# Kernel optimization log

Hardware: AMD Instinct MI355X
Metric: run time of the kernel (lower is better)

The kernel has to match this reference:

```python
import jax, jax.numpy as jnp
import numpy as np

N = 50000   # nodes
E = 800000  # edges (avg degree 16)
D0 = 256    # input feat dim
H1, D1 = 4, 64  # layer1 heads, per-head dim
H2, D2 = 4, 64  # layer2 heads, per-head dim
NEG_SLOPE = 0.2


def setup_inputs() -> dict:
    key = jax.random.key(0)
    ks = jax.random.split(key, 9)
    s = 0.1
    feature = jax.random.normal(ks[0], (N, D0), jnp.float32)
    src = jax.random.randint(ks[1], (E,), 0, N, dtype=jnp.int32)
    dst = jax.random.randint(ks[2], (E,), 0, N, dtype=jnp.int32)
    W1 = jax.random.normal(ks[3], (D0, H1 * D1), jnp.float32) * s
    al1 = jax.random.normal(ks[4], (H1, D1), jnp.float32) * s
    ar1 = jax.random.normal(ks[5], (H1, D1), jnp.float32) * s
    W2 = jax.random.normal(ks[6], (H1 * D1, H2 * D2), jnp.float32) * s
    al2 = jax.random.normal(ks[7], (H2, D2), jnp.float32) * s
    ar2 = jax.random.normal(ks[8], (H2, D2), jnp.float32) * s
    return dict(feature=feature, W1=W1, al1=al1, ar1=ar1,
                W2=W2, al2=al2, ar2=ar2, src=src, dst=dst)


def gat_conv(x, W, al, ar, src, dst, H, d, act):
    # x: [N, in]; W: [in, H*d]; al, ar: [H, d]
    feat = (x @ W).reshape(N, H, d)                 # [N,H,d]
    el = jnp.einsum('nhd,hd->nh', feat, al)         # [N,H] src-side score
    er = jnp.einsum('nhd,hd->nh', feat, ar)         # [N,H] dst-side score
    e = jax.nn.leaky_relu(el[src] + er[dst], NEG_SLOPE)  # [E,H]
    # segment softmax over edges grouped by destination node
    m = jax.ops.segment_max(e, dst, num_segments=N)      # [N,H]
    ex = jnp.exp(e - m[dst])                             # [E,H]
    denom = jax.ops.segment_sum(ex, dst, num_segments=N) # [N,H]
    alpha = ex / jnp.maximum(denom[dst], 1e-9)           # [E,H]
    msg = feat[src] * alpha[..., None]                   # [E,H,d]
    out = jax.ops.segment_sum(msg, dst, num_segments=N)  # [N,H,d]
    return act(out)


def reference(feature, W1, al1, ar1, W2, al2, ar2, src, dst):
    h = gat_conv(feature, W1, al1, ar1, src, dst, H1, D1, jax.nn.elu)  # [N,H1,D1]
    h = h.reshape(N, H1 * D1)                                          # concat heads
    h = gat_conv(h, W2, al2, ar2, src, dst, H2, D2, lambda x: x)       # [N,H2,D2]
    return h.mean(axis=1)                                              # mean over heads -> [N,D2]
```

## Files before the change

kernel.cpp:

```cpp
#include <hip/hip_runtime.h>
#include <hip/hip_fp16.h>
#include <math.h>
#include <stdint.h>

#define NNODES 50000
#define NEDGES 800000
#define DIM 256
#define HEADS 4
#define DH 64
#define NEG_SLOPE 0.2f

#define CSR_NPB 1024
#define CSR_NB ((NNODES + CSR_NPB - 1) / CSR_NPB)

typedef _Float16 half8 __attribute__((ext_vector_type(8)));
typedef float floatx4 __attribute__((ext_vector_type(4)));

static __device__ __forceinline__ float h2f(unsigned short h) {
  __half x = *(const __half*)&h;
  return __half2float(x);
}
static __device__ __forceinline__ unsigned short f2h(float f) {
  __half x = __float2half(f);
  return *(const unsigned short*)&x;
}

__global__ __launch_bounds__(256) void wt_k(const float* __restrict__ W1,
                                            const float* __restrict__ W2,
                                            _Float16* __restrict__ WT1,
                                            _Float16* __restrict__ WT2) {
  int b = blockIdx.x;
  const float* W = (b < 256) ? W1 : W2;
  _Float16* WT = (b < 256) ? WT1 : WT2;
  int n = b & 255;
  int k = threadIdx.x;
  WT[n * 256 + k] = (_Float16)W[k * 256 + n];
}

template <typename AT>
__global__ __launch_bounds__(256) void gemm_k(const AT* __restrict__ A,
                                              const _Float16* __restrict__ BT,
                                              const float* __restrict__ alw,
                                              const float* __restrict__ arw,
                                              unsigned short* __restrict__ Cb,
                                              float* __restrict__ el,
                                              float* __restrict__ er, int M) {
  __shared__ __attribute__((aligned(16))) _Float16 Asl[64][72];
  __shared__ __attribute__((aligned(16))) _Float16 Bsl[256][72];
  int t = threadIdx.x;
  int lane = t & 63, w = t >> 6;
  int m16 = lane & 15, q = lane >> 4;
  int row0 = blockIdx.x * 64;
  floatx4 acc[4][4];
#pragma unroll
  for (int i = 0; i < 4; ++i)
#pragma unroll
    for (int j = 0; j < 4; ++j) acc[i][j] = (floatx4){0.f, 0.f, 0.f, 0.f};

  float4 alv[4], arv[4];
#pragma unroll
  for (int ni = 0; ni < 4; ++ni) {
    alv[ni] = *(const float4*)&alw[w * 64 + ni * 16 + q * 4];
    arv[ni] = *(const float4*)&arw[w * 64 + ni * 16 + q * 4];
  }

  int arow = t >> 2, akoff = (t & 3) * 16;

  for (int k0 = 0; k0 < DIM; k0 += 64) {
    if constexpr (sizeof(AT) == 4) {
      float4 x0 = make_float4(0.f, 0.f, 0.f, 0.f), x1 = x0, x2 = x0, x3 = x0;
      if (row0 + arow < M) {
        const float* ap = (const float*)&A[(size_t)(row0 + arow) * DIM + k0 + akoff];
        x0 = *(const float4*)ap;
        x1 = *(const float4*)(ap + 4);
        x2 = *(const float4*)(ap + 8);
        x3 = *(const float4*)(ap + 12);
      }
      half8 h0, h1;
      h0[0] = (_Float16)x0.x; h0[1] = (_Float16)x0.y;
      h0[2] = (_Float16)x0.z; h0[3] = (_Float16)x0.w;
      h0[4] = (_Float16)x1.x; h0[5] = (_Float16)x1.y;
      h0[6] = (_Float16)x1.z; h0[7] = (_Float16)x1.w;
      h1[0] = (_Float16)x2.x; h1[1] = (_Float16)x2.y;
      h1[2] = (_Float16)x2.z; h1[3] = (_Float16)x2.w;
      h1[4] = (_Float16)x3.x; h1[5] = (_Float16)x3.y;
      h1[6] = (_Float16)x3.z; h1[7] = (_Float16)x3.w;
      *(half8*)&Asl[arow][akoff] = h0;
      *(half8*)&Asl[arow][akoff + 8] = h1;
    } else {
      int4 x0 = make_int4(0, 0, 0, 0), x1 = x0;
      if (row0 + arow < M) {
        const AT* ap = &A[(size_t)(row0 + arow) * DIM + k0 + akoff];
        x0 = *(const int4*)ap;
        x1 = *(const int4*)(ap + 8);
      }
      *(int4*)&Asl[arow][akoff] = x0;
      *(int4*)&Asl[arow][akoff + 8] = x1;
    }
    {
      const _Float16* bp = &BT[(size_t)t * 256 + k0];
#pragma unroll
      for (int c = 0; c < 8; ++c)
        *(int4*)&Bsl[t][c * 8] = *(const int4*)(bp + c * 8);
    }
    __syncthreads();
    half8 wf[2][4], af[2][4];
#pragma unroll
    for (int s = 0; s < 2; ++s)
#pragma unroll
      for (int i = 0; i < 4; ++i) {
        wf[s][i] = *(const half8*)&Bsl[w * 64 + i * 16 + m16][s * 32 + q * 8];
        af[s][i] = *(const half8*)&Asl[i * 16 + m16][s * 32 + q * 8];
      }
#pragma unroll
    for (int s = 0; s < 2; ++s)
#pragma unroll
      for (int mi = 0; mi < 4; ++mi)
#pragma unroll
        for (int ni = 0; ni < 4; ++ni)
          acc[mi][ni] = __builtin_amdgcn_mfma_f32_16x16x32_f16(
              wf[s][ni], af[s][mi], acc[mi][ni], 0, 0, 0);
    __syncthreads();
  }

#pragma unroll
  for (int mi = 0; mi < 4; ++mi) {
    int node = row0 + mi * 16 + m16;
    float pl = 0.f, pr = 0.f;
#pragma unroll
    for (int ni = 0; ni < 4; ++ni) {
      pl += acc[mi][ni][0] * alv[ni].x + acc[mi][ni][1] * alv[ni].y +
            acc[mi][ni][2] * alv[ni].z + acc[mi][ni][3] * alv[ni].w;
      pr += acc[mi][ni][0] * arv[ni].x + acc[mi][ni][1] * arv[ni].y +
            acc[mi][ni][2] * arv[ni].z + acc[mi][ni][3] * arv[ni].w;
    }
    pl += __shfl_xor(pl, 16, 64); pl += __shfl_xor(pl, 32, 64);
    pr += __shfl_xor(pr, 16, 64); pr += __shfl_xor(pr, 32, 64);
    if (q == 0 && node < M) {
      el[node * HEADS + w] = pl;
      er[node * HEADS + w] = pr;
    }
    if (node < M) {
#pragma unroll
      for (int ni = 0; ni < 4; ++ni) {
        ushort4 o;
        o.x = f2h(acc[mi][ni][0]); o.y = f2h(acc[mi][ni][1]);
        o.z = f2h(acc[mi][ni][2]); o.w = f2h(acc[mi][ni][3]);
        *(ushort4*)&Cb[(size_t)node * DIM + w * 64 + ni * 16 + q * 4] = o;
      }
    }
  }
}

__global__ __launch_bounds__(256) void deg_k(const int* __restrict__ dst,
                                             int* __restrict__ deg) {
  int e8 = (blockIdx.x * 256 + threadIdx.x) * 8;
  if (e8 < NEDGES) {
    int4 d0 = *(const int4*)&dst[e8];
    int4 d1 = *(const int4*)&dst[e8 + 4];
    atomicAdd(&deg[d0.x], 1);
    atomicAdd(&deg[d0.y], 1);
    atomicAdd(&deg[d0.z], 1);
    atomicAdd(&deg[d0.w], 1);
    atomicAdd(&deg[d1.x], 1);
    atomicAdd(&deg[d1.y], 1);
    atomicAdd(&deg[d1.z], 1);
    atomicAdd(&deg[d1.w], 1);
  }
}

__global__ __launch_bounds__(256) void csr_part_k(const int* __restrict__ deg,
                                                  int* __restrict__ bsum) {
  __shared__ int ws[4];
  int t = threadIdx.x, lane = t & 63, w = t >> 6;
  int idx = blockIdx.x * CSR_NPB + t * 4;
  int s = 0;
  if (idx < NNODES) {
    int4 v = *(const int4*)&deg[idx];
    s = v.x + v.y + v.z + v.w;
  }
#pragma unroll
  for (int off = 1; off < 64; off <<= 1) s += __shfl_xor(s, off, 64);
  if (lane == 0) ws[w] = s;
  __syncthreads();
  if (t == 0) bsum[blockIdx.x] = ws[0] + ws[1] + ws[2] + ws[3];
}

__global__ __launch_bounds__(64) void csr_mid_k(const int* __restrict__ bsum,
                                                int* __restrict__ bbase,
                                                int* __restrict__ row_ptr) {
  int t = threadIdx.x;
  int v = (t < CSR_NB) ? bsum[t] : 0;
  int incl = v;
#pragma unroll
  for (int off = 1; off < 64; off <<= 1) {
    int u = __shfl_up(incl, off, 64);
    if (t >= off) incl += u;
  }
  if (t < CSR_NB) bbase[t] = incl - v;
  if (t == 0) row_ptr[NNODES] = NEDGES;
}

__global__ __launch_bounds__(256) void csr_emit_k(const int* __restrict__ deg,
                                                  const int* __restrict__ bbase,
                                                  int* __restrict__ row_ptr,
                                                  int* __restrict__ cursor) {
  __shared__ int ws[4];
  int t = threadIdx.x, lane = t & 63, w = t >> 6;
  int idx = blockIdx.x * CSR_NPB + t * 4;
  int4 v = make_int4(0, 0, 0, 0);
  if (idx < NNODES) v = *(const int4*)&deg[idx];
  int s0 = v.x, s1 = s0 + v.y, s2 = s1 + v.z, s3 = s2 + v.w;
  int incl = s3;
#pragma unroll
  for (int off = 1; off < 64; off <<= 1) {
    int u = __shfl_up(incl, off, 64);
    if (lane >= off) incl += u;
  }
  if (lane == 63) ws[w] = incl;
  __syncthreads();
  int wbase = 0;
#pragma unroll
  for (int i = 0; i < 4; ++i)
    if (i < w) wbase += ws[i];
  int base = bbase[blockIdx.x] + wbase + incl - s3;
  if (idx < NNODES) {
    int4 rp = make_int4(base, base + s0, base + s1, base + s2);
    *(int4*)&row_ptr[idx] = rp;
    *(int4*)&cursor[idx] = rp;
  }
}

__global__ __launch_bounds__(256) void scatter_k(const int* __restrict__ src,
                                                 const int* __restrict__ dst,
                                                 int* __restrict__ cursor,
                                                 int* __restrict__ srcoff) {
  int e8 = (blockIdx.x * 256 + threadIdx.x) * 8;
  if (e8 < NEDGES) {
    int4 s0 = *(const int4*)&src[e8];
    int4 s1 = *(const int4*)&src[e8 + 4];
    int4 d0 = *(const int4*)&dst[e8];
    int4 d1 = *(const int4*)&dst[e8 + 4];
    int p0 = atomicAdd(&cursor[d0.x], 1);
    int p1 = atomicAdd(&cursor[d0.y], 1);
    int p2 = atomicAdd(&cursor[d0.z], 1);
    int p3 = atomicAdd(&cursor[d0.w], 1);
    int p4 = atomicAdd(&cursor[d1.x], 1);
    int p5 = atomicAdd(&cursor[d1.y], 1);
    int p6 = atomicAdd(&cursor[d1.z], 1);
    int p7 = atomicAdd(&cursor[d1.w], 1);
    srcoff[p0] = s0.x << 9;
    srcoff[p1] = s0.y << 9;
    srcoff[p2] = s0.z << 9;
    srcoff[p3] = s0.w << 9;
    srcoff[p4] = s1.x << 9;
    srcoff[p5] = s1.y << 9;
    srcoff[p6] = s1.z << 9;
    srcoff[p7] = s1.w << 9;
  }
}

template <int MODE>
__global__ __launch_bounds__(256) void agg_k(const unsigned short* __restrict__ feat,
                                             const float* __restrict__ el,
                                             const float* __restrict__ er,
                                             const int* __restrict__ row_ptr,
                                             const int* __restrict__ srcoff,
                                             void* __restrict__ outp) {
  int lane = threadIdx.x & 63;
  int w = threadIdx.x >> 6;
  int n = blockIdx.x * 4 + w;
  if (n >= NNODES) return;
  int h = lane >> 4;
  int hsel = lane & 3;
  int esel = lane >> 2;
  int beg = row_ptr[n], end = row_ptr[n + 1];
  float erv = er[n * HEADS + hsel];
  int laneByte = lane * 8;
  const char* fb = (const char*)feat;
  const char* elb = (const char*)el;
  float a0 = 0.f, a1 = 0.f, a2 = 0.f, a3 = 0.f, sume = 0.f;
  for (int c0 = beg; c0 < end; c0 += 16) {
    int soff = 0;
    if (lane < 16 && c0 + lane < end) soff = srcoff[c0 + lane];
    float av = 0.f;
    if (c0 + esel < end) {
      int sE = __shfl(soff, esel, 64);
      float elv = *(const float*)(elb + (sE >> 5) + hsel * 4);
      float v = elv + erv;
      v = v > 0.f ? v : NEG_SLOPE * v;
      av = __expf(v);
    }
#pragma unroll
    for (int j = 0; j < 16; ++j) {
      int sB = __shfl(soff, j, 64);
      float a = __shfl(av, 4 * j + h, 64);
      ushort4 u = *(const ushort4*)(fb + (sB + laneByte));
      a0 += h2f(u.x) * a;
      a1 += h2f(u.y) * a;
      a2 += h2f(u.z) * a;
      a3 += h2f(u.w) * a;
      sume += a;
    }
  }
  float inv = 1.f / fmaxf(sume, 1e-9f);
  a0 *= inv; a1 *= inv; a2 *= inv; a3 *= inv;
  if (MODE == 1) {
    a0 = a0 > 0.f ? a0 : (__expf(a0) - 1.f);
    a1 = a1 > 0.f ? a1 : (__expf(a1) - 1.f);
    a2 = a2 > 0.f ? a2 : (__expf(a2) - 1.f);
    a3 = a3 > 0.f ? a3 : (__expf(a3) - 1.f);
    ushort4 o;
    o.x = f2h(a0); o.y = f2h(a1); o.z = f2h(a2); o.w = f2h(a3);
    *(ushort4*)((char*)outp + (size_t)n * 512 + laneByte) = o;
  } else {
    a0 += __shfl_xor(a0, 16, 64); a0 += __shfl_xor(a0, 32, 64);
    a1 += __shfl_xor(a1, 16, 64); a1 += __shfl_xor(a1, 32, 64);
    a2 += __shfl_xor(a2, 16, 64); a2 += __shfl_xor(a2, 32, 64);
    a3 += __shfl_xor(a3, 16, 64); a3 += __shfl_xor(a3, 32, 64);
    if (lane < 16) {
      float4 o = make_float4(a0 * 0.25f, a1 * 0.25f, a2 * 0.25f, a3 * 0.25f);
      *(float4*)((float*)outp + (size_t)n * 64 + lane * 4) = o;
    }
  }
}

extern "C" void kernel_launch(void* const* d_in, const int* in_sizes, int n_in,
                              void* d_out, int out_size, void* d_ws, size_t ws_size,
                              hipStream_t stream) {
  const float* feature = (const float*)d_in[0];
  const float* W1 = (const float*)d_in[1];
  const float* al1 = (const float*)d_in[2];
  const float* ar1 = (const float*)d_in[3];
  const float* W2 = (const float*)d_in[4];
  const float* al2 = (const float*)d_in[5];
  const float* ar2 = (const float*)d_in[6];
  const int* src = (const int*)d_in[7];
  const int* dst = (const int*)d_in[8];
  float* out = (float*)d_out;

  uintptr_t p = (uintptr_t)d_ws;
  auto alloc = [&](size_t bytes) -> void* {
    uintptr_t cur = (p + 255) & ~(uintptr_t)255;
    p = cur + bytes;
    return (void*)cur;
  };
  unsigned short* featH = (unsigned short*)alloc((size_t)NNODES * DIM * 2);
  unsigned short* hidH  = (unsigned short*)alloc((size_t)NNODES * DIM * 2);
  _Float16* WT1 = (_Float16*)alloc((size_t)256 * 256 * 2);
  _Float16* WT2 = (_Float16*)alloc((size_t)256 * 256 * 2);
  float* el    = (float*)alloc((size_t)NNODES * HEADS * 4);
  float* er    = (float*)alloc((size_t)NNODES * HEADS * 4);
  int* deg     = (int*)alloc((size_t)NNODES * 4);
  int* row_ptr = (int*)alloc((size_t)(NNODES + 1) * 4);
  int* cursor  = (int*)alloc((size_t)NNODES * 4);
  int* srcoff  = (int*)alloc((size_t)NEDGES * 4);
  int* bsum    = (int*)alloc((size_t)CSR_NB * 4);
  int* bbase   = (int*)alloc((size_t)CSR_NB * 4);

  const int E8B = (NEDGES / 8 + 255) / 256;
  const int MB = (NNODES + 63) / 64;
  const int AB = (NNODES + 3) / 4;

  wt_k<<<512, 256, 0, stream>>>(W1, W2, WT1, WT2);
  hipMemsetAsync(deg, 0, (size_t)NNODES * 4, stream);
  deg_k<<<E8B, 256, 0, stream>>>(dst, deg);
  csr_part_k<<<CSR_NB, 256, 0, stream>>>(deg, bsum);
  csr_mid_k<<<1, 64, 0, stream>>>(bsum, bbase, row_ptr);
  csr_emit_k<<<CSR_NB, 256, 0, stream>>>(deg, bbase, row_ptr, cursor);
  scatter_k<<<E8B, 256, 0, stream>>>(src, dst, cursor, srcoff);

  gemm_k<float><<<MB, 256, 0, stream>>>(feature, WT1, al1, ar1, featH, el, er, NNODES);
  agg_k<1><<<AB, 256, 0, stream>>>(featH, el, er, row_ptr, srcoff, hidH);

  gemm_k<_Float16><<<MB, 256, 0, stream>>>((const _Float16*)hidH, WT2, al2, ar2,
                                           featH, el, er, NNODES);
  agg_k<2><<<AB, 256, 0, stream>>>(featH, el, er, row_ptr, srcoff, out);
}
```

Measured before the change: 356.5 us.

## Accumulate GAT aggregation in packed fp16 and process 32 edges per chunk

The aggregation kernel now accumulates weighted features in packed half2 registers using fp16 multiply-adds instead of converting each element to float. Attention weights are pre-scaled by 1/64 to limit fp16 overflow, and the scale is undone at normalization. The edge chunk grows from 16 to 32 edges, and the softmax denominator is computed with a single shuffle reduction per chunk. The goal is fewer conversion and FMA instructions plus more memory-level parallelism, at the cost of fp16 accumulation error over high-degree nodes.

```diff
diff --git a/kernel.cpp b/kernel.cpp
--- a/kernel.cpp
+++ b/kernel.cpp
@@ -14,15 +14,22 @@
 #define CSR_NB ((NNODES + CSR_NPB - 1) / CSR_NPB)
 
 typedef _Float16 half8 __attribute__((ext_vector_type(8)));
+typedef _Float16 half2_t __attribute__((ext_vector_type(2)));
 typedef float floatx4 __attribute__((ext_vector_type(4)));
 
-static __device__ __forceinline__ float h2f(unsigned short h) {
-  __half x = *(const __half*)&h;
-  return __half2float(x);
-}
 static __device__ __forceinline__ unsigned short f2h(float f) {
   __half x = __float2half(f);
   return *(const unsigned short*)&x;
+}
+static __device__ __forceinline__ half2_t i2h2(int v) {
+  union { int i; half2_t h; } u;
+  u.i = v;
+  return u.h;
+}
+static __device__ __forceinline__ int h22i(half2_t h) {
+  union { half2_t h; int i; } u;
+  u.h = h;
+  return u.i;
 }
 
 __global__ __launch_bounds__(256) void wt_k(const float* __restrict__ W1,
@@ -279,32 +286,57 @@
   int laneByte = lane * 8;
   const char* fb = (const char*)feat;
   const char* elb = (const char*)el;
-  float a0 = 0.f, a1 = 0.f, a2 = 0.f, a3 = 0.f, sume = 0.f;
-  for (int c0 = beg; c0 < end; c0 += 16) {
+  const float SC = 0.015625f;
+  half2_t acc01 = (half2_t){(_Float16)0, (_Float16)0};
+  half2_t acc23 = (half2_t){(_Float16)0, (_Float16)0};
+  float sume_acc = 0.f;
+  for (int c0 = beg; c0 < end; c0 += 32) {
     int soff = 0;
-    if (lane < 16 && c0 + lane < end) soff = srcoff[c0 + lane];
-    float av = 0.f;
-    if (c0 + esel < end) {
-      int sE = __shfl(soff, esel, 64);
-      float elv = *(const float*)(elb + (sE >> 5) + hsel * 4);
-      float v = elv + erv;
-      v = v > 0.f ? v : NEG_SLOPE * v;
-      av = __expf(v);
-    }
-#pragma unroll
-    for (int j = 0; j < 16; ++j) {
+    if (lane < 32 && c0 + lane < end) soff = srcoff[c0 + lane];
+    float av0 = 0.f, av1 = 0.f;
+    {
+      int sE0 = __shfl(soff, esel, 64);
+      int sE1 = __shfl(soff, 16 + esel, 64);
+      if (c0 + esel < end) {
+        float elv = *(const float*)(elb + (sE0 >> 5) + hsel * 4);
+        float v = elv + erv;
+        v = v > 0.f ? v : NEG_SLOPE * v;
+        av0 = __expf(v);
+      }
+      if (c0 + 16 + esel < end) {
+        float elv = *(const float*)(elb + (sE1 >> 5) + hsel * 4);
+        float v = elv + erv;
+        v = v > 0.f ? v : NEG_SLOPE * v;
+        av1 = __expf(v);
+      }
+    }
+    _Float16 a0h = (_Float16)(av0 * SC);
+    _Float16 a1h = (_Float16)(av1 * SC);
+    int ah0 = h22i((half2_t){a0h, a0h});
+    int ah1 = h22i((half2_t){a1h, a1h});
+    float s = av0 + av1;
+    s += __shfl_xor(s, 4, 64);
+    s += __shfl_xor(s, 8, 64);
+    s += __shfl_xor(s, 16, 64);
+    s += __shfl_xor(s, 32, 64);
+    sume_acc += s;
+#pragma unroll
+    for (int j = 0; j < 32; ++j) {
       int sB = __shfl(soff, j, 64);
-      float a = __shfl(av, 4 * j + h, 64);
-      ushort4 u = *(const ushort4*)(fb + (sB + laneByte));
-      a0 += h2f(u.x) * a;
-      a1 += h2f(u.y) * a;
-      a2 += h2f(u.z) * a;
-      a3 += h2f(u.w) * a;
-      sume += a;
-    }
-  }
-  float inv = 1.f / fmaxf(sume, 1e-9f);
-  a0 *= inv; a1 *= inv; a2 *= inv; a3 *= inv;
+      int ai = (j < 16) ? __shfl(ah0, 4 * j + h, 64)
+                        : __shfl(ah1, 4 * (j - 16) + h, 64);
+      half2_t ah = i2h2(ai);
+      uint2 uv = *(const uint2*)(fb + (sB + laneByte));
+      acc01 += i2h2((int)uv.x) * ah;
+      acc23 += i2h2((int)uv.y) * ah;
+    }
+  }
+  float sume = __shfl(sume_acc, h, 64);
+  float inv = 64.0f / fmaxf(sume, 1e-9f);
+  float a0 = (float)acc01[0] * inv;
+  float a1 = (float)acc01[1] * inv;
+  float a2 = (float)acc23[0] * inv;
+  float a3 = (float)acc23[1] * inv;
   if (MODE == 1) {
     a0 = a0 > 0.f ? a0 : (__expf(a0) - 1.f);
     a1 = a1 > 0.f ? a1 : (__expf(a1) - 1.f);
```

Result: slower. 423.9 us (+18.9%).
